# Kernel tuning notes

Measured on AMD Instinct MI355X. Metric: run time of the kernel, lower is better.

Reference implementation:

```python
import jax, jax.numpy as jnp
import numpy as np

H = 4          # number of GCN heads (hard-coded self.h = 4)
EPS = 1e-6     # MWPToolkit LayerNorm eps
B, K, D, HID = 16, 1024, 256, 256
DK = D // H


def setup_inputs() -> dict:
    key = jax.random.key(0)
    ks = jax.random.split(key, 12)
    sc = lambda fan_in: 1.0 / np.sqrt(fan_in).astype(np.float32)
    return {
        "graph_nodes": jax.random.normal(ks[0], (B, K, D), jnp.float32),
        "graph": jax.random.randint(ks[1], (B, 5, K, K), 0, 2, jnp.int32),
        # per-head GCN layer 1: GraphConvolution(indim -> hiddim)
        "Wg1": jax.random.normal(ks[2], (H, D, HID), jnp.float32) * sc(D),
        "bg1": jax.random.normal(ks[3], (H, HID), jnp.float32) * sc(D),
        # per-head GCN layer 2: GraphConvolution(hiddim -> d_k)
        "Wg2": jax.random.normal(ks[4], (H, HID, DK), jnp.float32) * sc(HID),
        "bg2": jax.random.normal(ks[5], (H, DK), jnp.float32) * sc(HID),
        # PositionwiseFeedForward: Linear(indim,hiddim) -> ReLU -> Linear(hiddim,outdim)
        "Wf1": jax.random.normal(ks[6], (D, HID), jnp.float32) * sc(D),
        "bf1": jax.random.normal(ks[7], (HID,), jnp.float32) * sc(D),
        "Wf2": jax.random.normal(ks[8], (HID, D), jnp.float32) * sc(HID),
        "bf2": jax.random.normal(ks[9], (D,), jnp.float32) * sc(HID),
        # LayerNorm(outdim) affine params
        "ln_a": jnp.ones((D,), jnp.float32),
        "ln_b": jnp.zeros((D,), jnp.float32),
    }


def reference(graph_nodes, graph, Wg1, bg1, Wg2, bg2, Wf1, bf1, Wf2, bf2, ln_a, ln_b):
    adj = graph.astype(jnp.float32)                      # (B, 5, K, K)
    # adj_list = [adj[:,1], adj[:,1], adj[:,4], adj[:,4]] -> stack heads
    adj_h = jnp.stack([adj[:, 1], adj[:, 1], adj[:, 4], adj[:, 4]])  # (H,B,K,K)

    # GCN layer 1 (all heads at once): relu(adj @ (x @ W1) + b1)
    sup1 = jnp.einsum('bkd,hdf->hbkf', graph_nodes, Wg1)            # (H,B,K,HID)
    h1 = jax.nn.relu(jnp.einsum('hbkj,hbjf->hbkf', adj_h, sup1)
                     + bg1[:, None, None, :])
    # (dropout is identity in eval)
    # GCN layer 2: adj @ (h1 @ W2) + b2
    sup2 = jnp.einsum('hbkf,hfe->hbke', h1, Wg2)                    # (H,B,K,DK)
    h2 = jnp.einsum('hbkj,hbje->hbke', adj_h, sup2) + bg2[:, None, None, :]

    # concat heads along feature dim: (B,K,H*DK) == (B,K,D)
    g = jnp.transpose(h2, (1, 2, 0, 3)).reshape(h2.shape[1], h2.shape[2], -1)

    # MWPToolkit LayerNorm: a*(x-mean)/(std+eps)+b, std unbiased (ddof=1)
    mu = g.mean(-1, keepdims=True)
    sd = jnp.std(g, axis=-1, keepdims=True, ddof=1)
    g = ln_a * (g - mu) / (sd + EPS) + ln_b + graph_nodes           # residual

    # PositionwiseFeedForward + residual (dropout identity in eval)
    ff = jax.nn.relu(g @ Wf1 + bf1) @ Wf2 + bf2
    out = ff + g
    return adj, out
```

## Files before the change

kernel.cpp:

```cpp
#include <hip/hip_runtime.h>

typedef unsigned short ushort_t;
using short8  = __attribute__((ext_vector_type(8))) short;
using floatx4 = __attribute__((ext_vector_type(4))) float;

__device__ __forceinline__ ushort_t f2bf(float f) {
  unsigned int x = __builtin_bit_cast(unsigned int, f);
  x += 0x7fffu + ((x >> 16) & 1u);
  return (ushort_t)(x >> 16);
}

__device__ __forceinline__ void gld16(const ushort_t* g, ushort_t* l) {
  __builtin_amdgcn_global_load_lds(
      (const __attribute__((address_space(1))) void*)(unsigned long long)(uintptr_t)g,
      (__attribute__((address_space(3))) void*)l, 16, 0, 0);
}

template <typename F>
__device__ __forceinline__ void gemm_tile(const ushort_t* __restrict__ A, int lda,
                                          const ushort_t* __restrict__ BT, int ldb,
                                          int K, F epi) {
  __shared__ ushort_t As[128 * 64];
  __shared__ ushort_t Bs[128 * 64];

  const int tid  = threadIdx.x;
  const int wave = tid >> 6;
  const int lane = tid & 63;
  const int l15  = lane & 15;
  const int quad = lane >> 4;
  const int wm   = wave >> 1;
  const int wn   = wave & 1;

  const int srow8  = lane >> 3;
  const int schunk = lane & 7;
  const int gcol   = ((schunk ^ srow8) * 8);

  const ushort_t* gA = A  + (size_t)(wave * 32 + srow8) * lda + gcol;
  const ushort_t* gB = BT + (size_t)(wave * 32 + srow8) * ldb + gcol;
  ushort_t* lA = As + (wave * 32) * 64;
  ushort_t* lB = Bs + (wave * 32) * 64;

  floatx4 acc[4][4] = {};
  const int arow0 = (wm * 64 + l15) * 64;
  const int brow0 = (wn * 64 + l15) * 64;
  const int cx    = l15 & 7;

  for (int k0 = 0; k0 < K; k0 += 64) {
#pragma unroll
    for (int ci = 0; ci < 4; ci++) {
      gld16(gA + (size_t)(ci * 8) * lda, lA + ci * 512);
      gld16(gB + (size_t)(ci * 8) * ldb, lB + ci * 512);
    }
    gA += 64; gB += 64;
    __syncthreads();
#pragma unroll
    for (int ks = 0; ks < 2; ks++) {
      const int cs = ((ks * 4 + quad) ^ cx) * 8;
      short8 af[4], bfr[4];
#pragma unroll
      for (int i = 0; i < 4; i++) af[i]  = *(const short8*)(As + arow0 + i * 1024 + cs);
#pragma unroll
      for (int j = 0; j < 4; j++) bfr[j] = *(const short8*)(Bs + brow0 + j * 1024 + cs);
#pragma unroll
      for (int i = 0; i < 4; i++)
#pragma unroll
        for (int j = 0; j < 4; j++)
          acc[i][j] = __builtin_amdgcn_mfma_f32_16x16x32_bf16(af[i], bfr[j], acc[i][j], 0, 0, 0);
    }
    __syncthreads();
  }

#pragma unroll
  for (int i = 0; i < 4; i++)
#pragma unroll
    for (int j = 0; j < 4; j++)
#pragma unroll
      for (int r = 0; r < 4; r++)
        epi(wm * 64 + i * 16 + quad * 4 + r, wn * 64 + j * 16 + l15, acc[i][j][r]);
}

template <typename F>
__device__ __forceinline__ void gemm_tile_w(const ushort_t* __restrict__ A, int lda,
                                            const ushort_t* __restrict__ BT, int ldb,
                                            int K, F epi) {
  __shared__ ushort_t As[128 * 64];
  __shared__ ushort_t Bs[256 * 64];

  const int tid  = threadIdx.x;
  const int wave = tid >> 6;
  const int lane = tid & 63;
  const int l15  = lane & 15;
  const int quad = lane >> 4;
  const int wm   = wave >> 2;
  const int wn   = wave & 3;

  const int srow8  = lane >> 3;
  const int schunk = lane & 7;
  const int gcol   = ((schunk ^ srow8) * 8);

  const ushort_t* gA = A  + (size_t)(wave * 16 + srow8) * lda + gcol;
  const ushort_t* gB = BT + (size_t)(wave * 32 + srow8) * ldb + gcol;
  ushort_t* lA = As + (wave * 16) * 64;
  ushort_t* lB = Bs + (wave * 32) * 64;

  floatx4 acc[4][4] = {};
  const int arow0 = (wm * 64 + l15) * 64;
  const int brow0 = (wn * 64 + l15) * 64;
  const int cx    = l15 & 7;

  for (int k0 = 0; k0 < K; k0 += 64) {
#pragma unroll
    for (int ci = 0; ci < 2; ci++)
      gld16(gA + (size_t)(ci * 8) * lda, lA + ci * 512);
#pragma unroll
    for (int ci = 0; ci < 4; ci++)
      gld16(gB + (size_t)(ci * 8) * ldb, lB + ci * 512);
    gA += 64; gB += 64;
    __syncthreads();
#pragma unroll
    for (int ks = 0; ks < 2; ks++) {
      const int cs = ((ks * 4 + quad) ^ cx) * 8;
      short8 af[4], bfr[4];
#pragma unroll
      for (int i = 0; i < 4; i++) af[i]  = *(const short8*)(As + arow0 + i * 1024 + cs);
#pragma unroll
      for (int j = 0; j < 4; j++) bfr[j] = *(const short8*)(Bs + brow0 + j * 1024 + cs);
#pragma unroll
      for (int i = 0; i < 4; i++)
#pragma unroll
        for (int j = 0; j < 4; j++)
          acc[i][j] = __builtin_amdgcn_mfma_f32_16x16x32_bf16(af[i], bfr[j], acc[i][j], 0, 0, 0);
    }
    __syncthreads();
  }

#pragma unroll
  for (int i = 0; i < 4; i++)
#pragma unroll
    for (int j = 0; j < 4; j++)
#pragma unroll
      for (int r = 0; r < 4; r++)
        epi(wm * 64 + i * 16 + quad * 4 + r, wn * 64 + j * 16 + l15, acc[i][j][r]);
}


__global__ __launch_bounds__(256) void k_cast(const int* __restrict__ graph,
                                              float* __restrict__ adj_out,
                                              ushort_t* __restrict__ adjb) {
  const size_t i = (size_t)blockIdx.x * 256 + threadIdx.x;
  int4 v = ((const int4*)graph)[i];
  float4 f = make_float4((float)v.x, (float)v.y, (float)v.z, (float)v.w);
  ((float4*)adj_out)[i] = f;
  const size_t e0 = i * 4;
  const unsigned sb = (unsigned)(e0 >> 20);
  const unsigned s = sb % 5u, b = sb / 5u;
  if (s == 1u || s == 4u) {
    const unsigned tt = (s == 4u) ? 1u : 0u;
    ushort4 h;
    h.x = f2bf(f.x); h.y = f2bf(f.y); h.z = f2bf(f.z); h.w = f2bf(f.w);
    *(ushort4*)(adjb + (((size_t)(b * 2 + tt)) << 20) + (e0 & 0xFFFFFu)) = h;
  }
}

__global__ __launch_bounds__(256) void k_xt(const float* __restrict__ gn,
                                            ushort_t* __restrict__ XT) {
  __shared__ float t[64][68];
  const int b = blockIdx.z, dt = blockIdx.y, kt = blockIdx.x;
  const int r  = threadIdx.x >> 4;
  const int c4 = (threadIdx.x & 15) * 4;
#pragma unroll
  for (int rr = 0; rr < 4; rr++) {
    const int kl = rr * 16 + r;
    float4 v = *(const float4*)(gn + ((size_t)(b * 1024 + kt * 64 + kl)) * 256 + dt * 64 + c4);
    t[kl][c4] = v.x; t[kl][c4 + 1] = v.y; t[kl][c4 + 2] = v.z; t[kl][c4 + 3] = v.w;
  }
  __syncthreads();
#pragma unroll
  for (int rr = 0; rr < 4; rr++) {
    const int dl = rr * 16 + r;
    ushort4 h;
    h.x = f2bf(t[c4][dl]);     h.y = f2bf(t[c4 + 1][dl]);
    h.z = f2bf(t[c4 + 2][dl]); h.w = f2bf(t[c4 + 3][dl]);
    *(ushort4*)(XT + ((size_t)(b * 256 + dt * 64 + dl)) * 1024 + kt * 64 + c4) = h;
  }
}

__global__ __launch_bounds__(256) void k_prepw(const float* __restrict__ Wg1, const float* __restrict__ Wg2,
                                               const float* __restrict__ Wf1, const float* __restrict__ Wf2,
                                               ushort_t* __restrict__ W1T, ushort_t* __restrict__ W2pT,
                                               ushort_t* __restrict__ Wf1T, ushort_t* __restrict__ Wf2T) {
  const int i = blockIdx.x * 256 + threadIdx.x;
  if (i < 262144) {
    const int fI = i >> 8, d = i & 255;
    const int h = fI >> 8, ff = fI & 255;
    W1T[i] = f2bf(Wg1[((h << 8) + d) * 256 + ff]);
  } else if (i < 393216) {
    const int j = i - 262144;
    const int t = j >> 16, rem = j & 65535;
    const int ep = rem >> 9, k = rem & 511;
    const int hh = ep >> 6;
    const float v = ((k >> 8) == hh)
        ? Wg2[(((t * 2 + hh) << 8) + (k & 255)) * 64 + (ep & 63)] : 0.f;
    W2pT[j] = f2bf(v);
  } else if (i < 458752) {
    const int j = i - 393216;
    const int n = j >> 8, k = j & 255;
    Wf1T[j] = f2bf(Wf1[k * 256 + n]);
  } else if (i < 524288) {
    const int j = i - 458752;
    const int n = j >> 8, k = j & 255;
    Wf2T[j] = f2bf(Wf2[k * 256 + n]);
  }
}


__global__ __launch_bounds__(512) void k_ax(const ushort_t* __restrict__ adjb,
                                            const ushort_t* __restrict__ XT,
                                            ushort_t* __restrict__ AX) {
  const int mt = blockIdx.x, bt = blockIdx.y;
  const int b = bt >> 1;
  const ushort_t* A  = adjb + ((size_t)bt << 20) + (size_t)mt * 128 * 1024;
  const ushort_t* BT = XT + ((size_t)b << 18);
  ushort_t* C = AX + ((size_t)bt << 18);
  gemm_tile_w(A, 1024, BT, 1024, 1024, [&](int r, int c, float v) {
    C[(size_t)(mt * 128 + r) * 256 + c] = f2bf(v);
  });
}

__global__ __launch_bounds__(512) void k_h1(const ushort_t* __restrict__ AX,
                                            const ushort_t* __restrict__ W1T,
                                            const float* __restrict__ bg1,
                                            ushort_t* __restrict__ h1) {
  const int nt = blockIdx.x, mt = blockIdx.y, b = blockIdx.z;
  const int t = nt >> 1;
  const ushort_t* A  = AX + ((size_t)(b * 2 + t) << 18) + (size_t)mt * 128 * 256;
  const ushort_t* BT = W1T + ((size_t)nt << 16);
  ushort_t* C = h1 + ((size_t)b << 20);
  const float* bias = bg1 + nt * 256;
  gemm_tile_w(A, 256, BT, 256, 256, [&](int r, int c, float v) {
    C[(size_t)(mt * 128 + r) * 1024 + nt * 256 + c] = f2bf(fmaxf(v + bias[c], 0.f));
  });
}

__global__ __launch_bounds__(256) void k_g3(const ushort_t* __restrict__ W2pT,
                                            const ushort_t* __restrict__ h1,
                                            ushort_t* __restrict__ sup2T) {
  const int nt = blockIdx.x, bt = blockIdx.y;
  const int b = bt >> 1, t = bt & 1;
  const ushort_t* A  = W2pT + (size_t)t * 65536;
  const ushort_t* BT = h1 + ((size_t)b << 20) + (size_t)nt * 131072 + t * 512;
  ushort_t* C = sup2T + (size_t)bt * 131072;
  gemm_tile(A, 512, BT, 1024, 512, [&](int r, int c, float v) {
    C[(size_t)r * 1024 + nt * 128 + c] = f2bf(v);
  });
}

__global__ __launch_bounds__(256) void k_g4(const ushort_t* __restrict__ adjb,
                                            const ushort_t* __restrict__ sup2T,
                                            const float* __restrict__ bg2,
                                            float* __restrict__ g) {
  const int nt = blockIdx.x, mt = blockIdx.y, b = blockIdx.z;
  const ushort_t* A  = adjb + ((size_t)(b * 2 + nt) << 20) + (size_t)mt * 128 * 1024;
  const ushort_t* BT = sup2T + (size_t)(b * 2 + nt) * 131072;
  float* C = g + (size_t)b * 262144;
  const float* bias = bg2 + nt * 128;
  gemm_tile(A, 1024, BT, 1024, 1024, [&](int r, int c, float v) {
    C[(size_t)(mt * 128 + r) * 256 + nt * 128 + c] = v + bias[c];
  });
}

__global__ __launch_bounds__(256) void k_ln(const float* __restrict__ g, const float* __restrict__ gn,
                                            const float* __restrict__ la, const float* __restrict__ lb,
                                            float* __restrict__ glnf, ushort_t* __restrict__ glnb) {
  const int row = blockIdx.x * 4 + (threadIdx.x >> 6);
  const int lane = threadIdx.x & 63;
  const float4 x = ((const float4*)(g + (size_t)row * 256))[lane];
  float s = x.x + x.y + x.z + x.w;
#pragma unroll
  for (int o = 1; o < 64; o <<= 1) s += __shfl_xor(s, o);
  const float mu = s * (1.f / 256.f);
  const float dx = x.x - mu, dy = x.y - mu, dz = x.z - mu, dw = x.w - mu;
  float q = dx * dx + dy * dy + dz * dz + dw * dw;
#pragma unroll
  for (int o = 1; o < 64; o <<= 1) q += __shfl_xor(q, o);
  const float inv = 1.f / (sqrtf(q * (1.f / 255.f)) + 1e-6f);
  const float4 a  = ((const float4*)la)[lane];
  const float4 bb = ((const float4*)lb)[lane];
  const float4 rz = ((const float4*)(gn + (size_t)row * 256))[lane];
  float4 o;
  o.x = a.x * dx * inv + bb.x + rz.x;
  o.y = a.y * dy * inv + bb.y + rz.y;
  o.z = a.z * dz * inv + bb.z + rz.z;
  o.w = a.w * dw * inv + bb.w + rz.w;
  ((float4*)(glnf + (size_t)row * 256))[lane] = o;
  ushort4 h; h.x = f2bf(o.x); h.y = f2bf(o.y); h.z = f2bf(o.z); h.w = f2bf(o.w);
  ((ushort4*)(glnb + (size_t)row * 256))[lane] = h;
}

__global__ __launch_bounds__(256) void k_f1(const ushort_t* __restrict__ gln,
                                            const ushort_t* __restrict__ Wf1T,
                                            const float* __restrict__ bf1,
                                            ushort_t* __restrict__ tb) {
  const int nt = blockIdx.x, mt = blockIdx.y;
  const ushort_t* A  = gln + (size_t)mt * 128 * 256;
  const ushort_t* BT = Wf1T + (size_t)nt * 128 * 256;
  const float* bias = bf1 + nt * 128;
  gemm_tile(A, 256, BT, 256, 256, [&](int r, int c, float v) {
    tb[(size_t)(mt * 128 + r) * 256 + nt * 128 + c] = f2bf(fmaxf(v + bias[c], 0.f));
  });
}

__global__ __launch_bounds__(256) void k_f2(const ushort_t* __restrict__ tb,
                                            const ushort_t* __restrict__ Wf2T,
                                            const float* __restrict__ bf2,
                                            const float* __restrict__ glnf,
                                            float* __restrict__ out) {
  const int nt = blockIdx.x, mt = blockIdx.y;
  const ushort_t* A  = tb + (size_t)mt * 128 * 256;
  const ushort_t* BT = Wf2T + (size_t)nt * 128 * 256;
  const float* bias = bf2 + nt * 128;
  gemm_tile(A, 256, BT, 256, 256, [&](int r, int c, float v) {
    const size_t idx = (size_t)(mt * 128 + r) * 256 + nt * 128 + c;
    out[idx] = v + bias[c] + glnf[idx];
  });
}

extern "C" void kernel_launch(void* const* d_in, const int* in_sizes, int n_in,
                              void* d_out, int out_size, void* d_ws, size_t ws_size,
                              hipStream_t stream) {
  const float* gnodes = (const float*)d_in[0];
  const int*   graph  = (const int*)d_in[1];
  const float* Wg1 = (const float*)d_in[2];
  const float* bg1 = (const float*)d_in[3];
  const float* Wg2 = (const float*)d_in[4];
  const float* bg2 = (const float*)d_in[5];
  const float* Wf1 = (const float*)d_in[6];
  const float* bf1 = (const float*)d_in[7];
  const float* Wf2 = (const float*)d_in[8];
  const float* bf2 = (const float*)d_in[9];
  const float* ln_a = (const float*)d_in[10];
  const float* ln_b = (const float*)d_in[11];

  float* adj_out = (float*)d_out;
  float* out     = (float*)d_out + 83886080;

  char* ws = (char*)d_ws;
  ushort_t* adjb  = (ushort_t*)(ws);
  ushort_t* XT    = (ushort_t*)(ws + 67108864);
  ushort_t* W1T   = (ushort_t*)(ws + 75497472);
  ushort_t* W2pT  = (ushort_t*)(ws + 76021760);
  ushort_t* Wf1T  = (ushort_t*)(ws + 76283904);
  ushort_t* Wf2T  = (ushort_t*)(ws + 76414976);
  ushort_t* AX    = (ushort_t*)(ws + 76546048);
  ushort_t* h1    = (ushort_t*)(ws + 93323264);
  ushort_t* sup2T = (ushort_t*)(ws + 126877696);
  float*    gbuf  = (float*)(ws + 135266304);
  float*    glnf  = (float*)(ws + 152043520);
  ushort_t* glnb  = (ushort_t*)(ws + 168820736);
  ushort_t* tbuf  = (ushort_t*)(ws + 177209344);

  k_xt   <<<dim3(16, 4, 16), 256, 0, stream>>>(gnodes, XT);
  k_prepw<<<2048, 256, 0, stream>>>(Wg1, Wg2, Wf1, Wf2, W1T, W2pT, Wf1T, Wf2T);
  k_cast <<<81920, 256, 0, stream>>>(graph, adj_out, adjb);

  k_ax<<<dim3(8, 32), 512, 0, stream>>>(adjb, XT, AX);
  k_h1<<<dim3(4, 8, 16), 512, 0, stream>>>(AX, W1T, bg1, h1);
  k_g3<<<dim3(8, 32), 256, 0, stream>>>(W2pT, h1, sup2T);
  k_g4<<<dim3(2, 8, 16), 256, 0, stream>>>(adjb, sup2T, bg2, gbuf);

  k_ln<<<4096, 256, 0, stream>>>(gbuf, gnodes, ln_a, ln_b, glnf, glnb);

  k_f1<<<dim3(2, 128), 256, 0, stream>>>(glnb, Wf1T, bf1, tbuf);
  k_f2<<<dim3(2, 128), 256, 0, stream>>>(tbuf, Wf2T, bf2, glnf, out);
}
```

Measured before the change: 712.6 us.

## Fuse second adjacency GEMM with LayerNorm and retile GCN GEMMs to 128x128

The second graph-aggregation GEMM now computes full 256-wide rows per block, so its epilogue can apply the bias and the LayerNorm (reduced through shared memory) and write only a bf16 normalized buffer. This removes the fp32 intermediate buffer, the separate LayerNorm kernel and the fp32 residual copy. k_ax and k_h1 switch from the 512-thread wide tile to the 256-thread 128x128 tile with more blocks. In exchange, the final residual is read from bf16, which loses precision, and the fused kernel uses 64-row tiles that load A less efficiently.

```diff
diff --git a/kernel.cpp b/kernel.cpp
--- a/kernel.cpp
+++ b/kernel.cpp
@@ -8,6 +8,10 @@
   unsigned int x = __builtin_bit_cast(unsigned int, f);
   x += 0x7fffu + ((x >> 16) & 1u);
   return (ushort_t)(x >> 16);
+}
+
+__device__ __forceinline__ float bf2f(ushort_t h) {
+  return __builtin_bit_cast(float, (unsigned int)h << 16);
 }
 
 __device__ __forceinline__ void gld16(const ushort_t* g, ushort_t* l) {
@@ -51,70 +55,6 @@
       gld16(gA + (size_t)(ci * 8) * lda, lA + ci * 512);
       gld16(gB + (size_t)(ci * 8) * ldb, lB + ci * 512);
     }
-    gA += 64; gB += 64;
-    __syncthreads();
-#pragma unroll
-    for (int ks = 0; ks < 2; ks++) {
-      const int cs = ((ks * 4 + quad) ^ cx) * 8;
-      short8 af[4], bfr[4];
-#pragma unroll
-      for (int i = 0; i < 4; i++) af[i]  = *(const short8*)(As + arow0 + i * 1024 + cs);
-#pragma unroll
-      for (int j = 0; j < 4; j++) bfr[j] = *(const short8*)(Bs + brow0 + j * 1024 + cs);
-#pragma unroll
-      for (int i = 0; i < 4; i++)
-#pragma unroll
-        for (int j = 0; j < 4; j++)
-          acc[i][j] = __builtin_amdgcn_mfma_f32_16x16x32_bf16(af[i], bfr[j], acc[i][j], 0, 0, 0);
-    }
-    __syncthreads();
-  }
-
-#pragma unroll
-  for (int i = 0; i < 4; i++)
-#pragma unroll
-    for (int j = 0; j < 4; j++)
-#pragma unroll
-      for (int r = 0; r < 4; r++)
-        epi(wm * 64 + i * 16 + quad * 4 + r, wn * 64 + j * 16 + l15, acc[i][j][r]);
-}
-
-template <typename F>
-__device__ __forceinline__ void gemm_tile_w(const ushort_t* __restrict__ A, int lda,
-                                            const ushort_t* __restrict__ BT, int ldb,
-                                            int K, F epi) {
-  __shared__ ushort_t As[128 * 64];
-  __shared__ ushort_t Bs[256 * 64];
-
-  const int tid  = threadIdx.x;
-  const int wave = tid >> 6;
-  const int lane = tid & 63;
-  const int l15  = lane & 15;
-  const int quad = lane >> 4;
-  const int wm   = wave >> 2;
-  const int wn   = wave & 3;
-
-  const int srow8  = lane >> 3;
-  const int schunk = lane & 7;
-  const int gcol   = ((schunk ^ srow8) * 8);
-
-  const ushort_t* gA = A  + (size_t)(wave * 16 + srow8) * lda + gcol;
-  const ushort_t* gB = BT + (size_t)(wave * 32 + srow8) * ldb + gcol;
-  ushort_t* lA = As + (wave * 16) * 64;
-  ushort_t* lB = Bs + (wave * 32) * 64;
-
-  floatx4 acc[4][4] = {};
-  const int arow0 = (wm * 64 + l15) * 64;
-  const int brow0 = (wn * 64 + l15) * 64;
-  const int cx    = l15 & 7;
-
-  for (int k0 = 0; k0 < K; k0 += 64) {
-#pragma unroll
-    for (int ci = 0; ci < 2; ci++)
-      gld16(gA + (size_t)(ci * 8) * lda, lA + ci * 512);
-#pragma unroll
-    for (int ci = 0; ci < 4; ci++)
-      gld16(gB + (size_t)(ci * 8) * ldb, lB + ci * 512);
     gA += 64; gB += 64;
     __syncthreads();
 #pragma unroll
@@ -214,31 +154,31 @@
 }
 
 
-__global__ __launch_bounds__(512) void k_ax(const ushort_t* __restrict__ adjb,
+__global__ __launch_bounds__(256) void k_ax(const ushort_t* __restrict__ adjb,
                                             const ushort_t* __restrict__ XT,
                                             ushort_t* __restrict__ AX) {
-  const int mt = blockIdx.x, bt = blockIdx.y;
+  const int nt = blockIdx.x, mt = blockIdx.y, bt = blockIdx.z;
   const int b = bt >> 1;
   const ushort_t* A  = adjb + ((size_t)bt << 20) + (size_t)mt * 128 * 1024;
-  const ushort_t* BT = XT + ((size_t)b << 18);
+  const ushort_t* BT = XT + ((size_t)b << 18) + (size_t)nt * 128 * 1024;
   ushort_t* C = AX + ((size_t)bt << 18);
-  gemm_tile_w(A, 1024, BT, 1024, 1024, [&](int r, int c, float v) {
-    C[(size_t)(mt * 128 + r) * 256 + c] = f2bf(v);
-  });
-}
-
-__global__ __launch_bounds__(512) void k_h1(const ushort_t* __restrict__ AX,
+  gemm_tile(A, 1024, BT, 1024, 1024, [&](int r, int c, float v) {
+    C[(size_t)(mt * 128 + r) * 256 + nt * 128 + c] = f2bf(v);
+  });
+}
+
+__global__ __launch_bounds__(256) void k_h1(const ushort_t* __restrict__ AX,
                                             const ushort_t* __restrict__ W1T,
                                             const float* __restrict__ bg1,
                                             ushort_t* __restrict__ h1) {
   const int nt = blockIdx.x, mt = blockIdx.y, b = blockIdx.z;
-  const int t = nt >> 1;
+  const int t = nt >> 2;
   const ushort_t* A  = AX + ((size_t)(b * 2 + t) << 18) + (size_t)mt * 128 * 256;
-  const ushort_t* BT = W1T + ((size_t)nt << 16);
+  const ushort_t* BT = W1T + (size_t)nt * 128 * 256;
   ushort_t* C = h1 + ((size_t)b << 20);
-  const float* bias = bg1 + nt * 256;
-  gemm_tile_w(A, 256, BT, 256, 256, [&](int r, int c, float v) {
-    C[(size_t)(mt * 128 + r) * 1024 + nt * 256 + c] = f2bf(fmaxf(v + bias[c], 0.f));
+  const float* bias = bg1 + nt * 128;
+  gemm_tile(A, 256, BT, 256, 256, [&](int r, int c, float v) {
+    C[(size_t)(mt * 128 + r) * 1024 + nt * 128 + c] = f2bf(fmaxf(v + bias[c], 0.f));
   });
 }
 
@@ -255,46 +195,119 @@
   });
 }
 
-__global__ __launch_bounds__(256) void k_g4(const ushort_t* __restrict__ adjb,
-                                            const ushort_t* __restrict__ sup2T,
-                                            const float* __restrict__ bg2,
-                                            float* __restrict__ g) {
-  const int nt = blockIdx.x, mt = blockIdx.y, b = blockIdx.z;
-  const ushort_t* A  = adjb + ((size_t)(b * 2 + nt) << 20) + (size_t)mt * 128 * 1024;
-  const ushort_t* BT = sup2T + (size_t)(b * 2 + nt) * 131072;
-  float* C = g + (size_t)b * 262144;
-  const float* bias = bg2 + nt * 128;
-  gemm_tile(A, 1024, BT, 1024, 1024, [&](int r, int c, float v) {
-    C[(size_t)(mt * 128 + r) * 256 + nt * 128 + c] = v + bias[c];
-  });
-}
-
-__global__ __launch_bounds__(256) void k_ln(const float* __restrict__ g, const float* __restrict__ gn,
-                                            const float* __restrict__ la, const float* __restrict__ lb,
-                                            float* __restrict__ glnf, ushort_t* __restrict__ glnb) {
-  const int row = blockIdx.x * 4 + (threadIdx.x >> 6);
-  const int lane = threadIdx.x & 63;
-  const float4 x = ((const float4*)(g + (size_t)row * 256))[lane];
-  float s = x.x + x.y + x.z + x.w;
-#pragma unroll
-  for (int o = 1; o < 64; o <<= 1) s += __shfl_xor(s, o);
-  const float mu = s * (1.f / 256.f);
-  const float dx = x.x - mu, dy = x.y - mu, dz = x.z - mu, dw = x.w - mu;
-  float q = dx * dx + dy * dy + dz * dz + dw * dw;
-#pragma unroll
-  for (int o = 1; o < 64; o <<= 1) q += __shfl_xor(q, o);
-  const float inv = 1.f / (sqrtf(q * (1.f / 255.f)) + 1e-6f);
-  const float4 a  = ((const float4*)la)[lane];
-  const float4 bb = ((const float4*)lb)[lane];
-  const float4 rz = ((const float4*)(gn + (size_t)row * 256))[lane];
-  float4 o;
-  o.x = a.x * dx * inv + bb.x + rz.x;
-  o.y = a.y * dy * inv + bb.y + rz.y;
-  o.z = a.z * dz * inv + bb.z + rz.z;
-  o.w = a.w * dw * inv + bb.w + rz.w;
-  ((float4*)(glnf + (size_t)row * 256))[lane] = o;
-  ushort4 h; h.x = f2bf(o.x); h.y = f2bf(o.y); h.z = f2bf(o.z); h.w = f2bf(o.w);
-  ((ushort4*)(glnb + (size_t)row * 256))[lane] = h;
+__global__ __launch_bounds__(256) void k_g4ln(const ushort_t* __restrict__ adjb,
+                                              const ushort_t* __restrict__ sup2T,
+                                              const float* __restrict__ bg2,
+                                              const float* __restrict__ gn,
+                                              const float* __restrict__ la,
+                                              const float* __restrict__ lb,
+                                              ushort_t* __restrict__ glnb) {
+  __shared__ ushort_t As[128 * 64];
+  __shared__ ushort_t Bs[256 * 64];
+  __shared__ float sred[4][64], qred[4][64];
+
+  const int mt = blockIdx.x, b = blockIdx.y;
+  const int tid = threadIdx.x, wave = tid >> 6, lane = tid & 63;
+  const int l15 = lane & 15, quad = lane >> 4;
+  const int wn = wave;
+  const int tsel = wn >> 1;
+
+  const int srow8 = lane >> 3, schunk = lane & 7;
+  const int gcol = (schunk ^ srow8) * 8;
+
+  const ushort_t* adjt = adjb + ((size_t)(b * 2 + tsel) << 20) + (size_t)(mt * 64) * 1024;
+  const ushort_t* gA = adjt + (size_t)((wave & 1) * 32 + srow8) * 1024 + gcol;
+  const ushort_t* supt = sup2T + (size_t)(b * 2 + tsel) * 131072;
+  const ushort_t* gB = supt + (size_t)((wave & 1) * 64 + srow8) * 1024 + gcol;
+  ushort_t* lA = As + (wave * 32) * 64;
+  ushort_t* lB = Bs + (wave * 64) * 64;
+
+  floatx4 acc[4][4] = {};
+  const int arow0 = (tsel * 64 + l15) * 64;
+  const int brow0 = (wn * 64 + l15) * 64;
+  const int cx = l15 & 7;
+
+  for (int k0 = 0; k0 < 1024; k0 += 64) {
+#pragma unroll
+    for (int ci = 0; ci < 4; ci++)
+      gld16(gA + (size_t)(ci * 8) * 1024, lA + ci * 512);
+#pragma unroll
+    for (int ci = 0; ci < 8; ci++)
+      gld16(gB + (size_t)(ci * 8) * 1024, lB + ci * 512);
+    gA += 64; gB += 64;
+    __syncthreads();
+#pragma unroll
+    for (int ks = 0; ks < 2; ks++) {
+      const int cs = ((ks * 4 + quad) ^ cx) * 8;
+      short8 af[4], bfr[4];
+#pragma unroll
+      for (int i = 0; i < 4; i++) af[i]  = *(const short8*)(As + arow0 + i * 1024 + cs);
+#pragma unroll
+      for (int j = 0; j < 4; j++) bfr[j] = *(const short8*)(Bs + brow0 + j * 1024 + cs);
+#pragma unroll
+      for (int i = 0; i < 4; i++)
+#pragma unroll
+        for (int j = 0; j < 4; j++)
+          acc[i][j] = __builtin_amdgcn_mfma_f32_16x16x32_bf16(af[i], bfr[j], acc[i][j], 0, 0, 0);
+    }
+    __syncthreads();
+  }
+
+  float laj[4], lbj[4];
+#pragma unroll
+  for (int j = 0; j < 4; j++) {
+    const int colg = wn * 64 + j * 16 + l15;
+    const float bj = bg2[colg];
+    laj[j] = la[colg]; lbj[j] = lb[colg];
+#pragma unroll
+    for (int i = 0; i < 4; i++)
+#pragma unroll
+      for (int r = 0; r < 4; r++) acc[i][j][r] += bj;
+  }
+
+  float sv[4][4], qv[4][4];
+#pragma unroll
+  for (int i = 0; i < 4; i++)
+#pragma unroll
+    for (int r = 0; r < 4; r++) {
+      float s = 0.f, q = 0.f;
+#pragma unroll
+      for (int j = 0; j < 4; j++) { const float v = acc[i][j][r]; s += v; q += v * v; }
+#pragma unroll
+      for (int m = 1; m < 16; m <<= 1) { s += __shfl_xor(s, m); q += __shfl_xor(q, m); }
+      sv[i][r] = s; qv[i][r] = q;
+    }
+  if (l15 == 0) {
+#pragma unroll
+    for (int i = 0; i < 4; i++)
+#pragma unroll
+      for (int r = 0; r < 4; r++) {
+        const int row = i * 16 + quad * 4 + r;
+        sred[wn][row] = sv[i][r]; qred[wn][row] = qv[i][r];
+      }
+  }
+  __syncthreads();
+
+  const size_t rowbase = (size_t)(b * 1024 + mt * 64);
+#pragma unroll
+  for (int i = 0; i < 4; i++)
+#pragma unroll
+    for (int r = 0; r < 4; r++) {
+      const int row = i * 16 + quad * 4 + r;
+      const float S = sred[0][row] + sred[1][row] + sred[2][row] + sred[3][row];
+      const float Q = qred[0][row] + qred[1][row] + qred[2][row] + qred[3][row];
+      const float mu = S * (1.f / 256.f);
+      const float var = fmaxf((Q - S * mu) * (1.f / 255.f), 0.f);
+      const float inv = 1.f / (sqrtf(var) + 1e-6f);
+      const float* gnr = gn + (rowbase + row) * 256;
+      ushort_t* outr = glnb + (rowbase + row) * 256;
+#pragma unroll
+      for (int j = 0; j < 4; j++) {
+        const int colg = wn * 64 + j * 16 + l15;
+        const float o = laj[j] * (acc[i][j][r] - mu) * inv + lbj[j] + gnr[colg];
+        outr[colg] = f2bf(o);
+      }
+    }
 }
 
 __global__ __launch_bounds__(256) void k_f1(const ushort_t* __restrict__ gln,
@@ -313,7 +326,7 @@
 __global__ __launch_bounds__(256) void k_f2(const ushort_t* __restrict__ tb,
                                             const ushort_t* __restrict__ Wf2T,
                                             const float* __restrict__ bf2,
-                                            const float* __restrict__ glnf,
+                                            const ushort_t* __restrict__ glnb,
                                             float* __restrict__ out) {
   const int nt = blockIdx.x, mt = blockIdx.y;
   const ushort_t* A  = tb + (size_t)mt * 128 * 256;
@@ -321,7 +334,7 @@
   const float* bias = bf2 + nt * 128;
   gemm_tile(A, 256, BT, 256, 256, [&](int r, int c, float v) {
     const size_t idx = (size_t)(mt * 128 + r) * 256 + nt * 128 + c;
-    out[idx] = v + bias[c] + glnf[idx];
+    out[idx] = v + bias[c] + bf2f(glnb[idx]);
   });
 }
 
@@ -354,22 +367,18 @@
   ushort_t* AX    = (ushort_t*)(ws + 76546048);
   ushort_t* h1    = (ushort_t*)(ws + 93323264);
   ushort_t* sup2T = (ushort_t*)(ws + 126877696);
-  float*    gbuf  = (float*)(ws + 135266304);
-  float*    glnf  = (float*)(ws + 152043520);
-  ushort_t* glnb  = (ushort_t*)(ws + 168820736);
-  ushort_t* tbuf  = (ushort_t*)(ws + 177209344);
+  ushort_t* glnb  = (ushort_t*)(ws + 135266304);
+  ushort_t* tbuf  = (ushort_t*)(ws + 143654912);
 
   k_xt   <<<dim3(16, 4, 16), 256, 0, stream>>>(gnodes, XT);
   k_prepw<<<2048, 256, 0, stream>>>(Wg1, Wg2, Wf1, Wf2, W1T, W2pT, Wf1T, Wf2T);
   k_cast <<<81920, 256, 0, stream>>>(graph, adj_out, adjb);
 
-  k_ax<<<dim3(8, 32), 512, 0, stream>>>(adjb, XT, AX);
-  k_h1<<<dim3(4, 8, 16), 512, 0, stream>>>(AX, W1T, bg1, h1);
+  k_ax<<<dim3(2, 8, 32), 256, 0, stream>>>(adjb, XT, AX);
+  k_h1<<<dim3(8, 8, 16), 256, 0, stream>>>(AX, W1T, bg1, h1);
   k_g3<<<dim3(8, 32), 256, 0, stream>>>(W2pT, h1, sup2T);
-  k_g4<<<dim3(2, 8, 16), 256, 0, stream>>>(adjb, sup2T, bg2, gbuf);
-
-  k_ln<<<4096, 256, 0, stream>>>(gbuf, gnodes, ln_a, ln_b, glnf, glnb);
+  k_g4ln<<<dim3(16, 16), 256, 0, stream>>>(adjb, sup2T, bg2, gnodes, ln_a, ln_b, glnb);
 
   k_f1<<<dim3(2, 128), 256, 0, stream>>>(glnb, Wf1T, bf1, tbuf);
-  k_f2<<<dim3(2, 128), 256, 0, stream>>>(tbuf, Wf2T, bf2, glnf, out);
-}
+  k_f2<<<dim3(2, 128), 256, 0, stream>>>(tbuf, Wf2T, bf2, glnb, out);
+}
```

New measurement: 710.5 us. No clear change (-0.3%).
